# Kernel tuning notes

Hardware: AMD Instinct MI355X
Metric: run time of the kernel (lower is better)

The kernel has to match this reference:

```python
import jax, jax.numpy as jnp
import numpy as np

# Fixed 3x3 gaussian kernel from the original module (not learned)
_KERNEL = jnp.array([[0.03797616, 0.044863533, 0.03797616],
                     [0.044863533, 0.053,      0.044863533],
                     [0.03797616, 0.044863533, 0.03797616]], dtype=jnp.float32)


def _gaussian_con(x):
    # torch expands kernel to (C_out=C, C_in=C, 3, 3): every output channel is the
    # gaussian filter applied to the SUM over input channels (cross-channel mixing).
    C = x.shape[1]
    w = jnp.broadcast_to(_KERNEL, (C, C, 3, 3)).astype(x.dtype)
    return jax.lax.conv_general_dilated(
        x, w, window_strides=(1, 1), padding='SAME',
        dimension_numbers=('NCHW', 'OIHW', 'NCHW'))


def setup_inputs() -> dict:
    key = jax.random.key(0)
    k1, k2 = jax.random.split(key)
    B, C, H, W = 8, 3, 1024, 1024
    x = jax.random.uniform(k1, (B, C, H, W), dtype=jnp.float32)
    y = jax.random.uniform(k2, (B, C, H, W), dtype=jnp.float32)
    return {"x": x, "y": y}


def reference(x, y):
    B, C, W, H = x.shape  # original names x.size()[2]=width, [3]=heigh
    C1 = (0.01 * 255) ** 2
    C2 = (0.03 * 255) ** 2
    N = W * H  # pixels per channel
    denom = 3.0 * (N - 1)  # count starts at -1 in the original, then *3

    def step(carry, idx):
        xc, yc = carry
        # Original re-convolves the WHOLE batch each iteration (x = gaussion_con(x))
        xc = _gaussian_con(xc)
        yc = _gaussian_con(yc)
        xi = xc[idx]  # (3, W, H)
        yi = yc[idx]
        # mean over channels of per-channel means == global mean (equal-size channels)
        mean_x = xi.mean()
        mean_y = yi.mean()
        # unbiased (ddof=1) per-channel variance, averaged over the 3 channels
        std_x = jnp.var(xi, axis=(1, 2), ddof=1).mean()
        std_y = jnp.var(yi, axis=(1, 2), ddof=1).mean()
        # covariance-like term uses the GLOBAL means, summed over all channels/pixels
        conv = jnp.sum((xi - mean_x) * (yi - mean_y)) / denom
        one_turn = ((2 * mean_x * mean_y + C1) * (2 * conv + C2)) / (
            (mean_x ** 2 + mean_y ** 2 + C1) * (std_x ** 2 + std_y ** 2 + C2))
        return (xc, yc), one_turn

    (_, _), terms = jax.lax.scan(step, (x, y), jnp.arange(B))
    return terms.sum()
```

## Files before the change

### kernel.cpp

```cpp
#include <hip/hip_runtime.h>


typedef float v2f __attribute__((ext_vector_type(2)));
typedef float v4f __attribute__((ext_vector_type(4)));

#define BSTR 50

#define PC 0.19487473f
#define QC 0.23021731f

struct WtTables { float w[8][153]; };
static constexpr WtTables make_tables() {
  WtTables t{};
  for (int H = 1; H <= 8; ++H) {
    const int T = 2 * H + 1;
    for (int d = 0; d <= H; ++d) {
      float Wd[17] = {};
      for (int k = 0; k < T; ++k) Wd[k] = (k == H) ? 1.f : 0.f;
      const int kmin = H - d;
      for (int m = 0; m < H; ++m) {
        float prev = 0.f;
        for (int k = kmin; k < T; ++k) {
          const float cur = Wd[k];
          const float nxt = (k < T - 1) ? Wd[k + 1] : 0.f;
          Wd[k] = QC * cur + PC * (prev + nxt);
          prev = cur;
        }
      }
      for (int k = 0; k < T; ++k) t.w[H - 1][d * T + k] = Wd[k];
    }
  }
  return t;
}
__constant__ WtTables WTAB = make_tables();

struct SharedMem {
  v2f buf[48 * BSTR];
  double wred[4 * 5];
  float Wt[153];
};

__global__ __launch_bounds__(256) void ssim_zero(double* acc) {
  for (int i = threadIdx.x; i < 8 * 64 * 5; i += 256) acc[i] = 0.0;
}

template <int H>
__device__ __forceinline__ void body(SharedMem& sm, int oy, int ox, int tr, int tc,
                                     const float* __restrict__ xp,
                                     const float* __restrict__ yp,
                                     double* __restrict__ accn, int useStore) {
  constexpr int T = 2 * H + 1;
  constexpr int n = H - 1;
  constexpr int R0 = 8 - H, R1 = 39 + H;
  const int tid = threadIdx.x;
  const bool rowEdge = (tr == 0) | (tr == 31);
  const bool colEdge = (tc == 0) | (tc == 31);

  {
    constexpr int CC0 = (8 - H) >> 2, CC1 = (39 + H) >> 2;
    const size_t base = (size_t)n * 3145728u;
    auto doChunk = [&](int c) {
      const int row = c / 12;
      const int c4 = c - row * 12;
      if (row < R0 || row > R1 || c4 < CC0 || c4 > CC1) return;
      const int gy = oy + row - 8;
      const int gx0 = ox + c4 * 4 - 8;
      v4f sx = {0.f, 0.f, 0.f, 0.f}, sy = {0.f, 0.f, 0.f, 0.f};
      if (((unsigned)gy < 1024u) && ((unsigned)gx0 < 1024u)) {
        const size_t off = base + (size_t)gy * 1024u + (unsigned)gx0;
        const v4f* px = (const v4f*)(xp + off);
        const v4f* py = (const v4f*)(yp + off);
        sx = px[0] + px[262144] + px[524288];
        sy = py[0] + py[262144] + py[524288];
      }
      v4f* d = (v4f*)(sm.buf + row * BSTR + c4 * 4);
      d[0] = (v4f){sx.x, sy.x, sx.y, sy.y};
      d[1] = (v4f){sx.z, sy.z, sx.w, sy.w};
    };
    doChunk(tid);
    doChunk(tid + 256);
    if (tid < 64) doChunk(tid + 512);
  }
  if (rowEdge | colEdge) {
    for (int i = tid; i < (H + 1) * T; i += 256) sm.Wt[i] = WTAB.w[n][i];
  }
  __syncthreads();

  {
    const int g = tid >> 6;
    const int i0 = tid & 63;
    constexpr int I0 = (8 - H) >> 1, I1 = (15 + H) >> 1;
    const bool val = (i0 >= R0) & (i0 <= R1);
    v2f o[8] = {};
    if (val) {
      const v4f* s4 = (const v4f*)(sm.buf + i0 * BSTR + g * 8);
      v2f win[24];
#pragma unroll
      for (int i = I0; i <= I1; ++i) {
        const v4f t = s4[i];
        win[2 * i] = (v2f){t.x, t.y};
        win[2 * i + 1] = (v2f){t.z, t.w};
      }
      if (!colEdge) {
#pragma unroll
        for (int k = 0; k < T; ++k) {
          const float cw = WTAB.w[n][H * T + k];
#pragma unroll
          for (int j = 0; j < 8; ++j)
            o[j] += cw * win[j + k + 8 - H];
        }
      } else {
        int A0[8], sg[8];
#pragma unroll
        for (int j = 0; j < 8; ++j) {
          const int gx = ox + g * 8 + j;
          int dd = H, rv = 0;
          if (gx < H) dd = gx;
          else if (gx > 1023 - H) { dd = 1023 - gx; rv = 1; }
          A0[j] = dd * T + (rv ? 2 * H : 0);
          sg[j] = rv ? -1 : 1;
        }
#pragma unroll
        for (int j = 0; j < 8; ++j)
          for (int k = 0; k < T; ++k)
            o[j] += sm.Wt[A0[j] + sg[j] * k] * win[j + k + 8 - H];
      }
    }
    __syncthreads();
    if (val) {
      v4f* d = (v4f*)(sm.buf + i0 * BSTR + g * 8 + 8);
#pragma unroll
      for (int jj = 0; jj < 4; ++jj)
        d[jj] = (v4f){o[2 * jj].x, o[2 * jj].y, o[2 * jj + 1].x, o[2 * jj + 1].y};
    }
  }
  __syncthreads();

  constexpr float scales[8] = {1.f, 3.f, 9.f, 27.f, 81.f, 243.f, 729.f, 2187.f};
  const float scale = scales[n];
  float sA = 0.f, sB = 0.f, sAA = 0.f, sBB = 0.f, sAB = 0.f;
  {
    const int jt = tid & 31;
    const int iv = tid >> 5;
    constexpr int C0 = 8 - H, C1 = 11 + H;
    v2f vwin[20];
#pragma unroll
    for (int c = C0; c <= C1; ++c)
      vwin[c] = sm.buf[(4 * iv + c) * BSTR + 8 + jt];
    v2f o[4] = {};
    if (!rowEdge) {
#pragma unroll
      for (int k = 0; k < T; ++k) {
        const float cw = WTAB.w[n][H * T + k];
#pragma unroll
        for (int rr = 0; rr < 4; ++rr)
          o[rr] += cw * vwin[rr + k + 8 - H];
      }
    } else {
#pragma unroll
      for (int rr = 0; rr < 4; ++rr) {
        const int gy = oy + 4 * iv + rr;
        int dd = H, rv = 0;
        if (gy < H) dd = gy;
        else if (gy > 1023 - H) { dd = 1023 - gy; rv = 1; }
        const int A0 = dd * T + (rv ? 2 * H : 0);
        const int s = rv ? -1 : 1;
        for (int k = 0; k < T; ++k)
          o[rr] += sm.Wt[A0 + s * k] * vwin[rr + k + 8 - H];
      }
    }
#pragma unroll
    for (int rr = 0; rr < 4; ++rr) {
      const float A = scale * o[rr].x;
      const float B = scale * o[rr].y;
      sA += A; sB += B;
      sAA += A * A; sBB += B * B; sAB += A * B;
    }
  }

  double v[5] = {(double)sA, (double)sB, (double)sAA, (double)sBB, (double)sAB};
#pragma unroll
  for (int off = 32; off > 0; off >>= 1) {
#pragma unroll
    for (int k = 0; k < 5; ++k) v[k] += __shfl_down(v[k], off, 64);
  }
  const int lane = tid & 63, wv = tid >> 6;
  if (lane == 0) {
#pragma unroll
    for (int k = 0; k < 5; ++k) sm.wred[wv * 5 + k] = v[k];
  }
  __syncthreads();
  if (tid == 0) {
    if (useStore) {
#pragma unroll
      for (int k = 0; k < 5; ++k)
        accn[k] = sm.wred[k] + sm.wred[5 + k] + sm.wred[10 + k] + sm.wred[15 + k];
    } else {
#pragma unroll
      for (int k = 0; k < 5; ++k)
        atomicAdd(&accn[k], sm.wred[k] + sm.wred[5 + k] + sm.wred[10 + k] + sm.wred[15 + k]);
    }
  }
}

__global__ __launch_bounds__(256, 5) void ssim_main(const float* __restrict__ xp,
                                                    const float* __restrict__ yp,
                                                    double* __restrict__ acc,
                                                    int nslot, int useStore) {
  __shared__ SharedMem sm;
  const int bid = blockIdx.x;
  const int n = bid >> 10;
  const int tile = bid & 1023;
  const int tc = tile & 31;
  const int tr = tile >> 5;
  const int oy = tr * 32;
  const int ox = tc * 32;
  const int slot = tile & (nslot - 1);
  double* accn = acc + (n * nslot + slot) * 5;
  switch (n) {
    case 0: body<1>(sm, oy, ox, tr, tc, xp, yp, accn, useStore); break;
    case 1: body<2>(sm, oy, ox, tr, tc, xp, yp, accn, useStore); break;
    case 2: body<3>(sm, oy, ox, tr, tc, xp, yp, accn, useStore); break;
    case 3: body<4>(sm, oy, ox, tr, tc, xp, yp, accn, useStore); break;
    case 4: body<5>(sm, oy, ox, tr, tc, xp, yp, accn, useStore); break;
    case 5: body<6>(sm, oy, ox, tr, tc, xp, yp, accn, useStore); break;
    case 6: body<7>(sm, oy, ox, tr, tc, xp, yp, accn, useStore); break;
    default: body<8>(sm, oy, ox, tr, tc, xp, yp, accn, useStore); break;
  }
}

__global__ __launch_bounds__(1024) void ssim_final(const double* __restrict__ acc,
                                                   float* __restrict__ out, int nslot) {
  __shared__ double wp[16][5];
  __shared__ double terms[8];
  const int tid = threadIdx.x;
  const int s = tid >> 7;
  const int l = tid & 127;
  double v[5] = {0.0, 0.0, 0.0, 0.0, 0.0};
  for (int slot = l; slot < nslot; slot += 128) {
    const double* p = acc + (size_t)(s * nslot + slot) * 5;
#pragma unroll
    for (int k = 0; k < 5; ++k) v[k] += p[k];
  }
#pragma unroll
  for (int off = 32; off > 0; off >>= 1) {
#pragma unroll
    for (int k = 0; k < 5; ++k) v[k] += __shfl_down(v[k], off, 64);
  }
  if ((tid & 63) == 0) {
#pragma unroll
    for (int k = 0; k < 5; ++k) wp[tid >> 6][k] = v[k];
  }
  __syncthreads();
  if (tid < 8) {
    double u[5];
#pragma unroll
    for (int k = 0; k < 5; ++k) u[k] = wp[2 * tid][k] + wp[2 * tid + 1][k];
    const double C1 = 6.5025;
    const double C2 = 58.5225;
    const double N = 1048576.0;
    const double mA = u[0] / N, mB = u[1] / N;
    const double varA = (u[2] - N * mA * mA) / (N - 1.0);
    const double varB = (u[3] - N * mB * mB) / (N - 1.0);
    const double cov  = (u[4] - N * mA * mB) / (N - 1.0);
    terms[tid] = ((2.0 * mA * mB + C1) * (2.0 * cov + C2)) /
                 ((mA * mA + mB * mB + C1) * (varA * varA + varB * varB + C2));
  }
  __syncthreads();
  if (tid == 0) {
    double tot = 0.0;
    for (int i = 0; i < 8; ++i) tot += terms[i];
    out[0] = (float)tot;
  }
}

extern "C" void kernel_launch(void* const* d_in, const int* in_sizes, int n_in,
                              void* d_out, int out_size, void* d_ws, size_t ws_size,
                              hipStream_t stream) {
  const float* x = (const float*)d_in[0];
  const float* y = (const float*)d_in[1];
  double* acc = (double*)d_ws;
  float* out = (float*)d_out;

  const size_t need = (size_t)8 * 1024 * 5 * sizeof(double);
  const int bigws = ws_size >= need;
  const int nslot = bigws ? 1024 : 64;

  if (!bigws) ssim_zero<<<1, 256, 0, stream>>>(acc);
  ssim_main<<<8192, 256, 0, stream>>>(x, y, acc, nslot, bigws);
  ssim_final<<<1, 1024, 0, stream>>>(acc, out, nslot);
}
```

Before: 246.9 us.

## Make blocks persistent over four tiles with double-buffered prefetch and paired batch indices

Each block now handles four tiles: two tiles for a low-H batch index and two for its paired high-H index (1+8, 2+7, ...), so work per block is balanced. The global loads for the next tile are issued into registers during the current tile's convolution and written to a second shared buffer, overlapping memory latency with compute. Edge weight tables for both indices are loaded once per block, and the partial-sum slots drop to 512. The cost is double shared memory, more live registers (launch bounds lowered to 4 waves), extra barriers and a smaller grid of 2048 blocks.

```diff
diff --git a/kernel.cpp b/kernel.cpp
--- a/kernel.cpp
+++ b/kernel.cpp
@@ -5,9 +5,9 @@
 typedef float v4f __attribute__((ext_vector_type(4)));
 
 #define BSTR 50
-
 #define PC 0.19487473f
 #define QC 0.23021731f
+#define NSLOT 512
 
 struct WtTables { float w[8][153]; };
 static constexpr WtTables make_tables() {
@@ -35,110 +35,132 @@
 __constant__ WtTables WTAB = make_tables();
 
 struct SharedMem {
-  v2f buf[48 * BSTR];
+  v2f buf[2][48 * BSTR];
   double wred[4 * 5];
-  float Wt[153];
+  float Wt[2][153];
 };
 
 __global__ __launch_bounds__(256) void ssim_zero(double* acc) {
   for (int i = threadIdx.x; i < 8 * 64 * 5; i += 256) acc[i] = 0.0;
 }
 
+struct Stage {
+  v4f x0, x1, x2, y0, y1, y2;
+  int row, c4;
+  bool ok;
+  __device__ __forceinline__ void issue(const float* __restrict__ xp,
+                                        const float* __restrict__ yp,
+                                        size_t base, int oy, int ox, int cell) {
+    row = cell / 12;
+    c4 = cell - row * 12;
+    const int gy = oy + row - 8, gx = ox + c4 * 4 - 8;
+    ok = ((unsigned)gy < 1024u) & ((unsigned)gx < 1024u);
+    if (ok) {
+      const size_t off = base + (size_t)gy * 1024u + (unsigned)gx;
+      const v4f* px = (const v4f*)(xp + off);
+      const v4f* py = (const v4f*)(yp + off);
+      x0 = px[0];      y0 = py[0];
+      x1 = px[262144]; y1 = py[262144];
+      x2 = px[524288]; y2 = py[524288];
+    }
+  }
+  __device__ __forceinline__ void write(v2f* buf) {
+    v4f sx = {0.f, 0.f, 0.f, 0.f}, sy = {0.f, 0.f, 0.f, 0.f};
+    if (ok) { sx = x0 + x1 + x2; sy = y0 + y1 + y2; }
+    v4f* d = (v4f*)(buf + row * BSTR + c4 * 4);
+    d[0] = (v4f){sx.x, sy.x, sx.y, sy.y};
+    d[1] = (v4f){sx.z, sy.z, sx.w, sy.w};
+  }
+};
+
+__device__ __forceinline__ void stage_full(v2f* buf, const float* __restrict__ xp,
+                                           const float* __restrict__ yp,
+                                           int n0, int tile) {
+  const int tid = threadIdx.x;
+  const size_t base = (size_t)n0 * 3145728u;
+  const int oy = (tile >> 5) * 32, ox = (tile & 31) * 32;
+  Stage a, b, c;
+  a.issue(xp, yp, base, oy, ox, tid);
+  b.issue(xp, yp, base, oy, ox, tid + 256);
+  a.write(buf);
+  b.write(buf);
+  if (tid < 64) { c.issue(xp, yp, base, oy, ox, tid + 512); c.write(buf); }
+}
+
 template <int H>
-__device__ __forceinline__ void body(SharedMem& sm, int oy, int ox, int tr, int tc,
-                                     const float* __restrict__ xp,
-                                     const float* __restrict__ yp,
-                                     double* __restrict__ accn, int useStore) {
+__device__ __forceinline__ void compute_tile(
+    SharedMem& sm, const int cur, const int hi, const int tile,
+    const bool hasNext, const int n2, const int tile2,
+    const float* __restrict__ xp, const float* __restrict__ yp, float (&s5)[5]) {
   constexpr int T = 2 * H + 1;
   constexpr int n = H - 1;
   constexpr int R0 = 8 - H, R1 = 39 + H;
   const int tid = threadIdx.x;
+  const int tr = tile >> 5, tc = tile & 31;
+  const int oy = tr * 32, ox = tc * 32;
   const bool rowEdge = (tr == 0) | (tr == 31);
   const bool colEdge = (tc == 0) | (tc == 31);
-
-  {
-    constexpr int CC0 = (8 - H) >> 2, CC1 = (39 + H) >> 2;
-    const size_t base = (size_t)n * 3145728u;
-    auto doChunk = [&](int c) {
-      const int row = c / 12;
-      const int c4 = c - row * 12;
-      if (row < R0 || row > R1 || c4 < CC0 || c4 > CC1) return;
-      const int gy = oy + row - 8;
-      const int gx0 = ox + c4 * 4 - 8;
-      v4f sx = {0.f, 0.f, 0.f, 0.f}, sy = {0.f, 0.f, 0.f, 0.f};
-      if (((unsigned)gy < 1024u) && ((unsigned)gx0 < 1024u)) {
-        const size_t off = base + (size_t)gy * 1024u + (unsigned)gx0;
-        const v4f* px = (const v4f*)(xp + off);
-        const v4f* py = (const v4f*)(yp + off);
-        sx = px[0] + px[262144] + px[524288];
-        sy = py[0] + py[262144] + py[524288];
-      }
-      v4f* d = (v4f*)(sm.buf + row * BSTR + c4 * 4);
-      d[0] = (v4f){sx.x, sy.x, sx.y, sy.y};
-      d[1] = (v4f){sx.z, sy.z, sx.w, sy.w};
-    };
-    doChunk(tid);
-    doChunk(tid + 256);
-    if (tid < 64) doChunk(tid + 512);
-  }
-  if (rowEdge | colEdge) {
-    for (int i = tid; i < (H + 1) * T; i += 256) sm.Wt[i] = WTAB.w[n][i];
-  }
-  __syncthreads();
-
-  {
-    const int g = tid >> 6;
-    const int i0 = tid & 63;
-    constexpr int I0 = (8 - H) >> 1, I1 = (15 + H) >> 1;
-    const bool val = (i0 >= R0) & (i0 <= R1);
-    v2f o[8] = {};
-    if (val) {
-      const v4f* s4 = (const v4f*)(sm.buf + i0 * BSTR + g * 8);
-      v2f win[24];
-#pragma unroll
-      for (int i = I0; i <= I1; ++i) {
-        const v4f t = s4[i];
-        win[2 * i] = (v2f){t.x, t.y};
-        win[2 * i + 1] = (v2f){t.z, t.w};
-      }
-      if (!colEdge) {
-#pragma unroll
-        for (int k = 0; k < T; ++k) {
-          const float cw = WTAB.w[n][H * T + k];
-#pragma unroll
-          for (int j = 0; j < 8; ++j)
-            o[j] += cw * win[j + k + 8 - H];
-        }
-      } else {
-        int A0[8], sg[8];
-#pragma unroll
-        for (int j = 0; j < 8; ++j) {
-          const int gx = ox + g * 8 + j;
-          int dd = H, rv = 0;
-          if (gx < H) dd = gx;
-          else if (gx > 1023 - H) { dd = 1023 - gx; rv = 1; }
-          A0[j] = dd * T + (rv ? 2 * H : 0);
-          sg[j] = rv ? -1 : 1;
-        }
-#pragma unroll
-        for (int j = 0; j < 8; ++j)
-          for (int k = 0; k < T; ++k)
-            o[j] += sm.Wt[A0[j] + sg[j] * k] * win[j + k + 8 - H];
-      }
-    }
-    __syncthreads();
-    if (val) {
-      v4f* d = (v4f*)(sm.buf + i0 * BSTR + g * 8 + 8);
-#pragma unroll
-      for (int jj = 0; jj < 4; ++jj)
-        d[jj] = (v4f){o[2 * jj].x, o[2 * jj].y, o[2 * jj + 1].x, o[2 * jj + 1].y};
-    }
-  }
-  __syncthreads();
-
-  constexpr float scales[8] = {1.f, 3.f, 9.f, 27.f, 81.f, 243.f, 729.f, 2187.f};
-  const float scale = scales[n];
-  float sA = 0.f, sB = 0.f, sAA = 0.f, sBB = 0.f, sAB = 0.f;
+  v2f* bufc = sm.buf[cur];
+  v2f* bufn = sm.buf[cur ^ 1];
+  const int oy2 = (tile2 >> 5) * 32, ox2 = (tile2 & 31) * 32;
+  const size_t base2 = (size_t)n2 * 3145728u;
+
+  Stage stA, stB, stC;
+  if (hasNext) stA.issue(xp, yp, base2, oy2, ox2, tid);
+
+  __syncthreads();
+
+  const int cg = tid >> 6;
+  const int i0 = tid & 63;
+  constexpr int I0 = (8 - H) >> 1, I1 = (15 + H) >> 1;
+  const bool val = (i0 >= R0) & (i0 <= R1);
+  v2f o[8] = {};
+  if (val) {
+    const v4f* s4 = (const v4f*)(bufc + i0 * BSTR + cg * 8);
+    v2f win[24];
+#pragma unroll
+    for (int i = I0; i <= I1; ++i) {
+      const v4f t = s4[i];
+      win[2 * i] = (v2f){t.x, t.y};
+      win[2 * i + 1] = (v2f){t.z, t.w};
+    }
+    if (!colEdge) {
+#pragma unroll
+      for (int k = 0; k < T; ++k) {
+        const float cw = WTAB.w[n][H * T + k];
+#pragma unroll
+        for (int j = 0; j < 8; ++j) o[j] += cw * win[j + k + 8 - H];
+      }
+    } else {
+      int A0[8], sg[8];
+#pragma unroll
+      for (int j = 0; j < 8; ++j) {
+        const int gx = ox + cg * 8 + j;
+        int dd = H, rv = 0;
+        if (gx < H) dd = gx;
+        else if (gx > 1023 - H) { dd = 1023 - gx; rv = 1; }
+        A0[j] = dd * T + (rv ? 2 * H : 0);
+        sg[j] = rv ? -1 : 1;
+      }
+#pragma unroll
+      for (int j = 0; j < 8; ++j)
+        for (int k = 0; k < T; ++k)
+          o[j] += sm.Wt[hi][A0[j] + sg[j] * k] * win[j + k + 8 - H];
+    }
+  }
+  if (hasNext) {
+    stA.write(bufn);
+    stB.issue(xp, yp, base2, oy2, ox2, tid + 256);
+  }
+  __syncthreads();
+  if (val) {
+    v4f* d = (v4f*)(bufc + i0 * BSTR + cg * 8 + 8);
+#pragma unroll
+    for (int q = 0; q < 4; ++q)
+      d[q] = (v4f){o[2 * q].x, o[2 * q].y, o[2 * q + 1].x, o[2 * q + 1].y};
+  }
+  __syncthreads();
+
   {
     const int jt = tid & 31;
     const int iv = tid >> 5;
@@ -146,15 +168,14 @@
     v2f vwin[20];
 #pragma unroll
     for (int c = C0; c <= C1; ++c)
-      vwin[c] = sm.buf[(4 * iv + c) * BSTR + 8 + jt];
-    v2f o[4] = {};
+      vwin[c] = bufc[(4 * iv + c) * BSTR + 8 + jt];
+    v2f o2[4] = {};
     if (!rowEdge) {
 #pragma unroll
       for (int k = 0; k < T; ++k) {
         const float cw = WTAB.w[n][H * T + k];
 #pragma unroll
-        for (int rr = 0; rr < 4; ++rr)
-          o[rr] += cw * vwin[rr + k + 8 - H];
+        for (int rr = 0; rr < 4; ++rr) o2[rr] += cw * vwin[rr + k + 8 - H];
       }
     } else {
 #pragma unroll
@@ -164,27 +185,39 @@
         if (gy < H) dd = gy;
         else if (gy > 1023 - H) { dd = 1023 - gy; rv = 1; }
         const int A0 = dd * T + (rv ? 2 * H : 0);
-        const int s = rv ? -1 : 1;
+        const int sg2 = rv ? -1 : 1;
         for (int k = 0; k < T; ++k)
-          o[rr] += sm.Wt[A0 + s * k] * vwin[rr + k + 8 - H];
-      }
-    }
+          o2[rr] += sm.Wt[hi][A0 + sg2 * k] * vwin[rr + k + 8 - H];
+      }
+    }
+    constexpr float scales[8] = {1.f, 3.f, 9.f, 27.f, 81.f, 243.f, 729.f, 2187.f};
+    constexpr float scale = scales[n];
 #pragma unroll
     for (int rr = 0; rr < 4; ++rr) {
-      const float A = scale * o[rr].x;
-      const float B = scale * o[rr].y;
-      sA += A; sB += B;
-      sAA += A * A; sBB += B * B; sAB += A * B;
-    }
-  }
-
-  double v[5] = {(double)sA, (double)sB, (double)sAA, (double)sBB, (double)sAB};
+      const float A = scale * o2[rr].x;
+      const float B = scale * o2[rr].y;
+      s5[0] += A; s5[1] += B;
+      s5[2] += A * A; s5[3] += B * B; s5[4] += A * B;
+    }
+  }
+  if (hasNext) {
+    stB.write(bufn);
+    if (tid < 64) { stC.issue(xp, yp, base2, oy2, ox2, tid + 512); stC.write(bufn); }
+  }
+}
+
+__device__ __forceinline__ void reduceStore(SharedMem& sm, const float (&s5)[5],
+                                            double* __restrict__ acc, int n0,
+                                            int slot, int useStore) {
+  double v[5];
+#pragma unroll
+  for (int k = 0; k < 5; ++k) v[k] = (double)s5[k];
 #pragma unroll
   for (int off = 32; off > 0; off >>= 1) {
 #pragma unroll
     for (int k = 0; k < 5; ++k) v[k] += __shfl_down(v[k], off, 64);
   }
-  const int lane = tid & 63, wv = tid >> 6;
+  const int tid = threadIdx.x, lane = tid & 63, wv = tid >> 6;
   if (lane == 0) {
 #pragma unroll
     for (int k = 0; k < 5; ++k) sm.wred[wv * 5 + k] = v[k];
@@ -192,40 +225,60 @@
   __syncthreads();
   if (tid == 0) {
     if (useStore) {
+      double* an = acc + (size_t)(n0 * NSLOT + slot) * 5;
 #pragma unroll
       for (int k = 0; k < 5; ++k)
-        accn[k] = sm.wred[k] + sm.wred[5 + k] + sm.wred[10 + k] + sm.wred[15 + k];
+        an[k] = sm.wred[k] + sm.wred[5 + k] + sm.wred[10 + k] + sm.wred[15 + k];
     } else {
+      double* an = acc + (size_t)(n0 * 64 + (slot & 63)) * 5;
 #pragma unroll
       for (int k = 0; k < 5; ++k)
-        atomicAdd(&accn[k], sm.wred[k] + sm.wred[5 + k] + sm.wred[10 + k] + sm.wred[15 + k]);
-    }
-  }
-}
-
-__global__ __launch_bounds__(256, 5) void ssim_main(const float* __restrict__ xp,
+        atomicAdd(&an[k], sm.wred[k] + sm.wred[5 + k] + sm.wred[10 + k] + sm.wred[15 + k]);
+    }
+  }
+  __syncthreads();
+}
+
+template <int HA, int HB>
+__device__ __forceinline__ void runBlock(SharedMem& sm, int h, int jj,
+                                         const float* __restrict__ xp,
+                                         const float* __restrict__ yp,
+                                         double* __restrict__ acc, int useStore) {
+  constexpr int nA = HA - 1, nB = HB - 1;
+  const int T0 = h * 512 + jj;
+  const int T1 = T0 + 256;
+  stage_full(sm.buf[0], xp, yp, nA, T0);
+
+  float s5[5] = {0.f, 0.f, 0.f, 0.f, 0.f};
+  compute_tile<HA>(sm, 0, 0, T0, true, nA, T1, xp, yp, s5);
+  compute_tile<HA>(sm, 1, 0, T1, true, nB, T0, xp, yp, s5);
+  reduceStore(sm, s5, acc, nA, h * 256 + jj, useStore);
+#pragma unroll
+  for (int k = 0; k < 5; ++k) s5[k] = 0.f;
+  compute_tile<HB>(sm, 0, 1, T0, true, nB, T1, xp, yp, s5);
+  compute_tile<HB>(sm, 1, 1, T1, false, 0, 0, xp, yp, s5);
+  reduceStore(sm, s5, acc, nB, h * 256 + jj, useStore);
+}
+
+__global__ __launch_bounds__(256, 4) void ssim_main(const float* __restrict__ xp,
                                                     const float* __restrict__ yp,
                                                     double* __restrict__ acc,
-                                                    int nslot, int useStore) {
+                                                    int useStore) {
   __shared__ SharedMem sm;
   const int bid = blockIdx.x;
-  const int n = bid >> 10;
-  const int tile = bid & 1023;
-  const int tc = tile & 31;
-  const int tr = tile >> 5;
-  const int oy = tr * 32;
-  const int ox = tc * 32;
-  const int slot = tile & (nslot - 1);
-  double* accn = acc + (n * nslot + slot) * 5;
-  switch (n) {
-    case 0: body<1>(sm, oy, ox, tr, tc, xp, yp, accn, useStore); break;
-    case 1: body<2>(sm, oy, ox, tr, tc, xp, yp, accn, useStore); break;
-    case 2: body<3>(sm, oy, ox, tr, tc, xp, yp, accn, useStore); break;
-    case 3: body<4>(sm, oy, ox, tr, tc, xp, yp, accn, useStore); break;
-    case 4: body<5>(sm, oy, ox, tr, tc, xp, yp, accn, useStore); break;
-    case 5: body<6>(sm, oy, ox, tr, tc, xp, yp, accn, useStore); break;
-    case 6: body<7>(sm, oy, ox, tr, tc, xp, yp, accn, useStore); break;
-    default: body<8>(sm, oy, ox, tr, tc, xp, yp, accn, useStore); break;
+  const int xcd = bid & 7;
+  const int jj = bid >> 3;
+  const int p = xcd >> 1;
+  const int h = xcd & 1;
+  for (int i = threadIdx.x; i < 153; i += 256) {
+    sm.Wt[0][i] = WTAB.w[p][i];
+    sm.Wt[1][i] = WTAB.w[7 - p][i];
+  }
+  switch (p) {
+    case 0:  runBlock<1, 8>(sm, h, jj, xp, yp, acc, useStore); break;
+    case 1:  runBlock<2, 7>(sm, h, jj, xp, yp, acc, useStore); break;
+    case 2:  runBlock<3, 6>(sm, h, jj, xp, yp, acc, useStore); break;
+    default: runBlock<4, 5>(sm, h, jj, xp, yp, acc, useStore); break;
   }
 }
 
@@ -282,11 +335,10 @@
   double* acc = (double*)d_ws;
   float* out = (float*)d_out;
 
-  const size_t need = (size_t)8 * 1024 * 5 * sizeof(double);
+  const size_t need = (size_t)8 * NSLOT * 5 * sizeof(double);
   const int bigws = ws_size >= need;
-  const int nslot = bigws ? 1024 : 64;
 
   if (!bigws) ssim_zero<<<1, 256, 0, stream>>>(acc);
-  ssim_main<<<8192, 256, 0, stream>>>(x, y, acc, nslot, bigws);
-  ssim_final<<<1, 1024, 0, stream>>>(acc, out, nslot);
-}
+  ssim_main<<<2048, 256, 0, stream>>>(x, y, acc, bigws);
+  ssim_final<<<1, 1024, 0, stream>>>(acc, out, bigws ? NSLOT : 64);
+}
```

New measurement: 240.0 us. 2.8% less time.
